# Kernel optimization log

Measured on AMD Instinct MI355X. Metric: run time of the kernel, lower is better.

Reference implementation:

```python
import jax, jax.numpy as jnp
import numpy as np

B, S, D, H, DH = 4, 2048, 1024, 16, 64

def setup_inputs() -> dict:
    key = jax.random.key(0)
    k1, k2, k3, k4, k5 = jax.random.split(key, 5)
    scale = 1.0 / np.sqrt(D)
    return {
        "x": jax.random.normal(k1, (B, S, D), dtype=jnp.float32),
        "w_qkv": jax.random.normal(k2, (D, 3, H, DH), dtype=jnp.float32) * scale,
        "b_qkv": jax.random.normal(k3, (3, H, DH), dtype=jnp.float32) * 0.02,
        "w_out": jax.random.normal(k4, (H, DH, D), dtype=jnp.float32) * (1.0 / np.sqrt(H * DH)),
        "b_out": jax.random.normal(k5, (D,), dtype=jnp.float32) * 0.02,
    }

def reference(x, w_qkv, b_qkv, w_out, b_out):
    # QKV projection: [B,S,D] x [D,3,H,Dh] -> [B,S,3,H,Dh]
    qkv = jnp.einsum('bsd,dthe->bsthe', x, w_qkv) + b_qkv
    q, k, v = qkv[:, :, 0], qkv[:, :, 1], qkv[:, :, 2]  # each [B,S,H,Dh]
    head_dim = q.shape[-1]
    # scores [B,H,Sq,Sk]
    scores = jnp.einsum('bqhe,bkhe->bhqk', q, k) / jnp.sqrt(jnp.float32(head_dim))
    seq = scores.shape[-1]
    causal = (jnp.arange(seq)[:, None] >= jnp.arange(seq)[None, :]).astype(scores.dtype)
    scores = scores - 1e9 * (1.0 - causal)  # additive mask as in source
    weights = jax.nn.softmax(scores, axis=-1)
    # dropout inactive (inference=True default)
    answers = jnp.einsum('bhqk,bkhe->bqhe', weights, v)  # [B,S,H,Dh]
    out = jnp.einsum('bqhe,hed->bqd', answers, w_out) + b_out
    return out
```

## Files before the change

kernel.cpp:

```cpp
#include <hip/hip_runtime.h>
#include <hip/hip_bf16.h>
#include <stdint.h>

#define B_    4
#define S_    2048
#define D_    1024
#define H_    16
#define DH_   64
#define M_TOT 8192
#define NQKV  3072
#define HDH   1024

typedef __bf16 bf16_t;
typedef bf16_t bf16x8 __attribute__((ext_vector_type(8)));
typedef float  f32x4  __attribute__((ext_vector_type(4)));
typedef float  f32x16 __attribute__((ext_vector_type(16)));

#define QSCALE 0.1803368801111204f

__device__ __forceinline__ short f2bf(float f) {
  union { float f; uint32_t u; } x; x.f = f;
  uint32_t r = (x.u + 0x7fffu + ((x.u >> 16) & 1u)) >> 16;
  return (short)(uint16_t)r;
}

__device__ __forceinline__ uint32_t cvt_pk_bf16(float lo, float hi) {
  uint32_t r;
  asm("v_cvt_pk_bf16_f32 %0, %1, %2" : "=v"(r) : "v"(lo), "v"(hi));
  return r;
}

__device__ __forceinline__ void permlane32_swap(uint32_t& d, uint32_t& s) {
  asm("v_permlane32_swap_b32 %0, %1" : "+v"(d), "+v"(s));
}

#define ASYNC_COPY16(g, l) \
  __builtin_amdgcn_global_load_lds((const __attribute__((address_space(1))) void*)(g), \
                                   (__attribute__((address_space(3))) void*)(l), 16, 0, 0)


__global__ __launch_bounds__(256) void k_cvt(const float* __restrict__ in, short* __restrict__ out, int n4) {
  int i = blockIdx.x * 256 + threadIdx.x;
  if (i < n4) {
    float4 v = ((const float4*)in)[i];
    short4 o;
    o.x = f2bf(v.x); o.y = f2bf(v.y); o.z = f2bf(v.z); o.w = f2bf(v.w);
    ((short4*)out)[i] = o;
  }
}

__global__ __launch_bounds__(256) void k_transpose_t(const float* __restrict__ in, short* __restrict__ out,
                                                     int R, int C) {
  __shared__ short t[32][33];
  const int bx = blockIdx.x * 32;
  const int by = blockIdx.y * 32;
  const int tid = threadIdx.x;
  const int row = tid >> 3, c4 = (tid & 7) * 4;
  const float4 v = *(const float4*)&in[(size_t)(by + row) * C + bx + c4];
  t[row][c4 + 0] = f2bf(v.x); t[row][c4 + 1] = f2bf(v.y);
  t[row][c4 + 2] = f2bf(v.z); t[row][c4 + 3] = f2bf(v.w);
  __syncthreads();
  short4 o;
  o.x = t[c4 + 0][row]; o.y = t[c4 + 1][row];
  o.z = t[c4 + 2][row]; o.w = t[c4 + 3][row];
  *(short4*)&out[(size_t)(bx + row) * R + by + c4] = o;
}


__device__ __forceinline__ void gemm_core(const short* __restrict__ A,
                                          const short* __restrict__ Bt,
                                          int row0, int col0, int K,
                                          short* lA, short* lB,
                                          f32x4 acc[4][4]) {
  const int tid  = threadIdx.x;
  const int wave = tid >> 6, lane = tid & 63;
  const int wr = wave >> 1, wc = wave & 1;
  const int stg_r = lane >> 2;
  const int stg_k = (lane & 3) * 8;
  const int fr = lane & 15;
  const int fk = (lane >> 4) * 8;

  for (int k0 = 0; k0 < K; k0 += 32) {
    __syncthreads();
#pragma unroll
    for (int c = 0; c < 2; ++c) {
      const int seg = wave * 2 + c;
      const short* ga = A  + (size_t)(row0 + seg * 16 + stg_r) * K + (k0 + stg_k);
      const short* gb = Bt + (size_t)(col0 + seg * 16 + stg_r) * K + (k0 + stg_k);
      ASYNC_COPY16(ga, lA + seg * 512);
      ASYNC_COPY16(gb, lB + seg * 512);
    }
    __syncthreads();
    bf16x8 af[4], bfr[4];
#pragma unroll
    for (int m = 0; m < 4; ++m)
      af[m] = *(const bf16x8*)(lA + (wr * 64 + m * 16 + fr) * 32 + fk);
#pragma unroll
    for (int n = 0; n < 4; ++n)
      bfr[n] = *(const bf16x8*)(lB + (wc * 64 + n * 16 + fr) * 32 + fk);
#pragma unroll
    for (int m = 0; m < 4; ++m)
#pragma unroll
      for (int n = 0; n < 4; ++n)
        acc[m][n] = __builtin_amdgcn_mfma_f32_16x16x32_bf16(af[m], bfr[n], acc[m][n], 0, 0, 0);
  }
}

__global__ __launch_bounds__(256) void k_gemm_qkv(const short* __restrict__ A, const short* __restrict__ Bt,
                                                  const float* __restrict__ bias,
                                                  short* __restrict__ Qb, short* __restrict__ Kb,
                                                  short* __restrict__ Vt) {
  __shared__ short lA[128 * 32];
  __shared__ short lB[128 * 32];
  f32x4 acc[4][4];
#pragma unroll
  for (int m = 0; m < 4; ++m)
#pragma unroll
    for (int n = 0; n < 4; ++n)
      acc[m][n] = (f32x4){0.f, 0.f, 0.f, 0.f};
  const int row0 = blockIdx.x * 128, col0 = blockIdx.y * 128;
  gemm_core(A, Bt, row0, col0, D_, lA, lB, acc);
  const int lane = threadIdx.x & 63, wave = threadIdx.x >> 6;
  const int wr = wave >> 1, wc = wave & 1;
#pragma unroll
  for (int m = 0; m < 4; ++m) {
    const int rbase = row0 + wr * 64 + m * 16 + (lane >> 4) * 4;
#pragma unroll
    for (int n = 0; n < 4; ++n) {
      const int col = col0 + wc * 64 + n * 16 + (lane & 15);
      const float bv = bias[col];
      const int t = col >> 10, rem = col & 1023, hh = rem >> 6, e = rem & 63;
#pragma unroll
      for (int r = 0; r < 4; ++r) {
        const int rw = rbase + r;
        const int bb = rw >> 11, s = rw & 2047;
        float v = acc[m][n][r] + bv;
        if (t == 0) {
          Qb[((size_t)(bb * H_ + hh) * S_ + s) * DH_ + e] = f2bf(v * QSCALE);
        } else if (t == 1) {
          Kb[((size_t)(bb * H_ + hh) * S_ + s) * DH_ + e] = f2bf(v);
        } else {
          Vt[((size_t)(bb * H_ + hh) * DH_ + e) * S_ + s] = f2bf(v);
        }
      }
    }
  }
}

__global__ __launch_bounds__(256) void k_gemm_out(const short* __restrict__ A, const short* __restrict__ Bt,
                                                  const float* __restrict__ bias, float* __restrict__ C) {
  __shared__ short lA[128 * 32];
  __shared__ short lB[128 * 32];
  f32x4 acc[4][4];
#pragma unroll
  for (int m = 0; m < 4; ++m)
#pragma unroll
    for (int n = 0; n < 4; ++n)
      acc[m][n] = (f32x4){0.f, 0.f, 0.f, 0.f};
  const int row0 = blockIdx.x * 128, col0 = blockIdx.y * 128;
  gemm_core(A, Bt, row0, col0, HDH, lA, lB, acc);
  const int lane = threadIdx.x & 63, wave = threadIdx.x >> 6;
  const int wr = wave >> 1, wc = wave & 1;
#pragma unroll
  for (int m = 0; m < 4; ++m) {
    const int rbase = row0 + wr * 64 + m * 16 + (lane >> 4) * 4;
#pragma unroll
    for (int n = 0; n < 4; ++n) {
      const int col = col0 + wc * 64 + n * 16 + (lane & 15);
      const float bv = bias[col];
#pragma unroll
      for (int r = 0; r < 4; ++r)
        C[(size_t)(rbase + r) * D_ + col] = acc[m][n][r] + bv;
    }
  }
}


template <bool MASKED>
__device__ __forceinline__ void softmax_pack(const f32x16& sacc, int ql, int hi,
                                             f32x16& o0, f32x16& o1,
                                             float& m, float& lsum,
                                             bf16x8& pb0v, bf16x8& pb1v) {
  float p[16];
#pragma unroll
  for (int r = 0; r < 16; ++r) {
    float s = sacc[r];
    if (MASKED) {
      const int kl = (r & 3) + 8 * (r >> 2) + 4 * hi;
      s = (kl <= ql) ? s : -1.0e30f;
    }
    p[r] = s;
  }
  float t0 = fmaxf(fmaxf(p[0], p[1]), p[2]);
  float t1 = fmaxf(fmaxf(p[3], p[4]), p[5]);
  float t2 = fmaxf(fmaxf(p[6], p[7]), p[8]);
  float t3 = fmaxf(fmaxf(p[9], p[10]), p[11]);
  float t4 = fmaxf(fmaxf(p[12], p[13]), p[14]);
  float pmax = fmaxf(fmaxf(fmaxf(t0, t1), t2), fmaxf(fmaxf(t3, t4), p[15]));
  if (__any(pmax - m > 8.0f)) {
    const float pmr = fmaxf(pmax, __shfl_xor(pmax, 32));
    const float mn = fmaxf(m, pmr);
    const float al = __builtin_amdgcn_exp2f(m - mn);
    lsum *= al;
#pragma unroll
    for (int r = 0; r < 16; ++r) { o0[r] *= al; o1[r] *= al; }
    m = mn;
  }
#pragma unroll
  for (int r = 0; r < 16; ++r) p[r] = __builtin_amdgcn_exp2f(p[r] - m);
  {
    float s0 = (p[0] + p[1]) + (p[2] + p[3]);
    float s1 = (p[4] + p[5]) + (p[6] + p[7]);
    float s2 = (p[8] + p[9]) + (p[10] + p[11]);
    float s3 = (p[12] + p[13]) + (p[14] + p[15]);
    lsum += (s0 + s1) + (s2 + s3);
  }
  uint32_t A0 = cvt_pk_bf16(p[0],  p[1]);
  uint32_t A1 = cvt_pk_bf16(p[2],  p[3]);
  uint32_t B0 = cvt_pk_bf16(p[4],  p[5]);
  uint32_t B1 = cvt_pk_bf16(p[6],  p[7]);
  uint32_t A2 = cvt_pk_bf16(p[8],  p[9]);
  uint32_t A3 = cvt_pk_bf16(p[10], p[11]);
  uint32_t B2 = cvt_pk_bf16(p[12], p[13]);
  uint32_t B3 = cvt_pk_bf16(p[14], p[15]);
  permlane32_swap(A0, B0);
  permlane32_swap(A1, B1);
  permlane32_swap(A2, B2);
  permlane32_swap(A3, B3);
  union { uint32_t u[4]; bf16x8 v; } pb0, pb1;
  pb0.u[0] = A0; pb0.u[1] = A1; pb0.u[2] = B0; pb0.u[3] = B1;
  pb1.u[0] = A2; pb1.u[1] = A3; pb1.u[2] = B2; pb1.u[3] = B3;
  pb0v = pb0.v; pb1v = pb1.v;
}

template <bool MASKED>
__device__ __forceinline__ void attn_tile(int kt, int ql, int hi,
                                          const short* __restrict__ Kp,
                                          const short* __restrict__ Vp,
                                          const bf16x8 qf[4],
                                          f32x16& oacc0, f32x16& oacc1,
                                          float& m, float& lsum) {
  const short* kb = Kp + (size_t)(kt + ql) * DH_ + hi * 8;
  bf16x8 kf0 = *(const bf16x8*)(kb);
  bf16x8 kf1 = *(const bf16x8*)(kb + 16);
  bf16x8 kf2 = *(const bf16x8*)(kb + 32);
  bf16x8 kf3 = *(const bf16x8*)(kb + 48);
  const short* vb0 = Vp + (size_t)(ql) * S_ + kt + hi * 8;
  const short* vb1 = Vp + (size_t)(32 + ql) * S_ + kt + hi * 8;
  bf16x8 vf00 = *(const bf16x8*)(vb0);
  bf16x8 vf01 = *(const bf16x8*)(vb0 + 16);
  bf16x8 vf10 = *(const bf16x8*)(vb1);
  bf16x8 vf11 = *(const bf16x8*)(vb1 + 16);

  f32x16 sacc;
#pragma unroll
  for (int r = 0; r < 16; ++r) sacc[r] = 0.f;
  __builtin_amdgcn_s_setprio(1);
  sacc = __builtin_amdgcn_mfma_f32_32x32x16_bf16(kf0, qf[0], sacc, 0, 0, 0);
  sacc = __builtin_amdgcn_mfma_f32_32x32x16_bf16(kf1, qf[1], sacc, 0, 0, 0);
  sacc = __builtin_amdgcn_mfma_f32_32x32x16_bf16(kf2, qf[2], sacc, 0, 0, 0);
  sacc = __builtin_amdgcn_mfma_f32_32x32x16_bf16(kf3, qf[3], sacc, 0, 0, 0);
  __builtin_amdgcn_s_setprio(0);

  bf16x8 pb0, pb1;
  softmax_pack<MASKED>(sacc, ql, hi, oacc0, oacc1, m, lsum, pb0, pb1);

  __builtin_amdgcn_s_setprio(1);
  oacc0 = __builtin_amdgcn_mfma_f32_32x32x16_bf16(vf00, pb0, oacc0, 0, 0, 0);
  oacc0 = __builtin_amdgcn_mfma_f32_32x32x16_bf16(vf01, pb1, oacc0, 0, 0, 0);
  oacc1 = __builtin_amdgcn_mfma_f32_32x32x16_bf16(vf10, pb0, oacc1, 0, 0, 0);
  oacc1 = __builtin_amdgcn_mfma_f32_32x32x16_bf16(vf11, pb1, oacc1, 0, 0, 0);
  __builtin_amdgcn_s_setprio(0);
}

template <bool MASKA>
__device__ __forceinline__ void attn_tile2(int kt, int ql, int hi,
                                           const short* __restrict__ Kp,
                                           const short* __restrict__ Vp,
                                           const bf16x8 qfA[4], const bf16x8 qfB[4],
                                           f32x16& oA0, f32x16& oA1, float& mA, float& lA,
                                           f32x16& oB0, f32x16& oB1, float& mB, float& lB) {
  const short* kb = Kp + (size_t)(kt + ql) * DH_ + hi * 8;
  bf16x8 kf0 = *(const bf16x8*)(kb);
  bf16x8 kf1 = *(const bf16x8*)(kb + 16);
  bf16x8 kf2 = *(const bf16x8*)(kb + 32);
  bf16x8 kf3 = *(const bf16x8*)(kb + 48);
  const short* vb0 = Vp + (size_t)(ql) * S_ + kt + hi * 8;
  const short* vb1 = Vp + (size_t)(32 + ql) * S_ + kt + hi * 8;
  bf16x8 vf00 = *(const bf16x8*)(vb0);
  bf16x8 vf01 = *(const bf16x8*)(vb0 + 16);
  bf16x8 vf10 = *(const bf16x8*)(vb1);
  bf16x8 vf11 = *(const bf16x8*)(vb1 + 16);

  f32x16 sA, sB;
#pragma unroll
  for (int r = 0; r < 16; ++r) { sA[r] = 0.f; sB[r] = 0.f; }
  __builtin_amdgcn_s_setprio(1);
  sA = __builtin_amdgcn_mfma_f32_32x32x16_bf16(kf0, qfA[0], sA, 0, 0, 0);
  sB = __builtin_amdgcn_mfma_f32_32x32x16_bf16(kf0, qfB[0], sB, 0, 0, 0);
  sA = __builtin_amdgcn_mfma_f32_32x32x16_bf16(kf1, qfA[1], sA, 0, 0, 0);
  sB = __builtin_amdgcn_mfma_f32_32x32x16_bf16(kf1, qfB[1], sB, 0, 0, 0);
  sA = __builtin_amdgcn_mfma_f32_32x32x16_bf16(kf2, qfA[2], sA, 0, 0, 0);
  sB = __builtin_amdgcn_mfma_f32_32x32x16_bf16(kf2, qfB[2], sB, 0, 0, 0);
  sA = __builtin_amdgcn_mfma_f32_32x32x16_bf16(kf3, qfA[3], sA, 0, 0, 0);
  sB = __builtin_amdgcn_mfma_f32_32x32x16_bf16(kf3, qfB[3], sB, 0, 0, 0);
  __builtin_amdgcn_s_setprio(0);

  bf16x8 pA0, pA1, pB0, pB1;
  softmax_pack<MASKA>(sA, ql, hi, oA0, oA1, mA, lA, pA0, pA1);
  softmax_pack<false>(sB, ql, hi, oB0, oB1, mB, lB, pB0, pB1);

  __builtin_amdgcn_s_setprio(1);
  oA0 = __builtin_amdgcn_mfma_f32_32x32x16_bf16(vf00, pA0, oA0, 0, 0, 0);
  oB0 = __builtin_amdgcn_mfma_f32_32x32x16_bf16(vf00, pB0, oB0, 0, 0, 0);
  oA0 = __builtin_amdgcn_mfma_f32_32x32x16_bf16(vf01, pA1, oA0, 0, 0, 0);
  oB0 = __builtin_amdgcn_mfma_f32_32x32x16_bf16(vf01, pB1, oB0, 0, 0, 0);
  oA1 = __builtin_amdgcn_mfma_f32_32x32x16_bf16(vf10, pA0, oA1, 0, 0, 0);
  oB1 = __builtin_amdgcn_mfma_f32_32x32x16_bf16(vf10, pB0, oB1, 0, 0, 0);
  oA1 = __builtin_amdgcn_mfma_f32_32x32x16_bf16(vf11, pA1, oA1, 0, 0, 0);
  oB1 = __builtin_amdgcn_mfma_f32_32x32x16_bf16(vf11, pB1, oB1, 0, 0, 0);
  __builtin_amdgcn_s_setprio(0);
}

__device__ __forceinline__ void write_out(short* __restrict__ att, int b, int h,
                                          int q0, int ql, int hi,
                                          const f32x16& o0, const f32x16& o1, float lsum) {
  lsum += __shfl_xor(lsum, 32);
  const float rl = __builtin_amdgcn_rcpf(lsum);
  short* ob = att + (size_t)((size_t)b * S_ + q0 + ql) * HDH + h * DH_ + 4 * hi;
#pragma unroll
  for (int dt = 0; dt < 2; ++dt) {
#pragma unroll
    for (int a = 0; a < 4; ++a) {
      const int rb = 4 * a;
      float v0 = (dt ? o1[rb + 0] : o0[rb + 0]) * rl;
      float v1 = (dt ? o1[rb + 1] : o0[rb + 1]) * rl;
      float v2 = (dt ? o1[rb + 2] : o0[rb + 2]) * rl;
      float v3 = (dt ? o1[rb + 3] : o0[rb + 3]) * rl;
      short4 o;
      o.x = f2bf(v0); o.y = f2bf(v1); o.z = f2bf(v2); o.w = f2bf(v3);
      *(short4*)(ob + dt * 32 + 8 * a) = o;
    }
  }
}

__global__ __launch_bounds__(64, 3) void k_attn(const short* __restrict__ Qb, const short* __restrict__ Kb,
                                                const short* __restrict__ Vt, short* __restrict__ att) {
  const int lane = threadIdx.x & 63;
  const int j = blockIdx.x;
  const int xcd = j & 7, c = j >> 3;
  const int bhLo = c & 7;
  const int s = 31 - (c >> 3);
  const int gg = xcd + 8 * bhLo;
  const int b = gg >> 4, h = gg & 15;
  const int pA = 2 * s, pB = 2 * s + 1;
  const int qA = pA * 32, qB = pB * 32;
  const size_t bh = (size_t)(b * H_ + h);
  const short* Qp = Qb + bh * (S_ * DH_);
  const short* Kp = Kb + bh * (S_ * DH_);
  const short* Vp = Vt + bh * (DH_ * S_);
  const int ql = lane & 31, hi = lane >> 5;

  bf16x8 qfA[4], qfB[4];
#pragma unroll
  for (int ss = 0; ss < 4; ++ss) {
    qfA[ss] = *(const bf16x8*)(Qp + (size_t)(qA + ql) * DH_ + ss * 16 + hi * 8);
    qfB[ss] = *(const bf16x8*)(Qp + (size_t)(qB + ql) * DH_ + ss * 16 + hi * 8);
  }

  f32x16 oA0, oA1, oB0, oB1;
#pragma unroll
  for (int r = 0; r < 16; ++r) { oA0[r] = 0.f; oA1[r] = 0.f; oB0[r] = 0.f; oB1[r] = 0.f; }
  float mA = -3.0e38f, lA = 0.f, mB = -3.0e38f, lB = 0.f;

#pragma unroll 1
  for (int t = 0; t < pA; ++t)
    attn_tile2<false>(t * 32, ql, hi, Kp, Vp, qfA, qfB, oA0, oA1, mA, lA, oB0, oB1, mB, lB);
  attn_tile2<true>(qA, ql, hi, Kp, Vp, qfA, qfB, oA0, oA1, mA, lA, oB0, oB1, mB, lB);
  attn_tile<true>(qB, ql, hi, Kp, Vp, qfB, oB0, oB1, mB, lB);

  write_out(att, b, h, qA, ql, hi, oA0, oA1, lA);
  write_out(att, b, h, qB, ql, hi, oB0, oB1, lB);
}


extern "C" void kernel_launch(void* const* d_in, const int* in_sizes, int n_in,
                              void* d_out, int out_size, void* d_ws, size_t ws_size,
                              hipStream_t stream) {
  const float* x     = (const float*)d_in[0];
  const float* w_qkv = (const float*)d_in[1];
  const float* b_qkv = (const float*)d_in[2];
  const float* w_out = (const float*)d_in[3];
  const float* b_out = (const float*)d_in[4];
  float* out = (float*)d_out;

  char* p = (char*)d_ws;
  short* xb    = (short*)p; p += (size_t)M_TOT * D_ * 2;
  short* wqkvT = (short*)p; p += (size_t)NQKV * D_ * 2;
  short* woutT = (short*)p; p += (size_t)D_ * HDH * 2;
  short* Qb    = (short*)p; p += (size_t)B_ * H_ * S_ * DH_ * 2;
  short* Kb    = (short*)p; p += (size_t)B_ * H_ * S_ * DH_ * 2;
  short* Vt    = (short*)p; p += (size_t)B_ * H_ * S_ * DH_ * 2;
  short* att   = (short*)p; p += (size_t)M_TOT * HDH * 2;

  k_cvt<<<M_TOT * D_ / 4 / 256, 256, 0, stream>>>(x, xb, M_TOT * D_ / 4);
  k_transpose_t<<<dim3(NQKV / 32, D_ / 32), 256, 0, stream>>>(w_qkv, wqkvT, D_, NQKV);
  k_transpose_t<<<dim3(D_ / 32, HDH / 32), 256, 0, stream>>>(w_out, woutT, HDH, D_);
  k_gemm_qkv<<<dim3(M_TOT / 128, NQKV / 128), 256, 0, stream>>>(xb, wqkvT, b_qkv, Qb, Kb, Vt);
  k_attn<<<2048, 64, 0, stream>>>(Qb, Kb, Vt, att);
  k_gemm_out<<<dim3(M_TOT / 128, D_ / 128), 256, 0, stream>>>(att, woutT, b_out, out);
}
```

Before: 202.9 us.

## Rewrite QKV GEMM with 256x256 tiles, double-buffered async LDS loads and swizzle

Replaces the QKV projection GEMM with a 512-thread kernel that computes 256x256 tiles using K-steps of 64. It double-buffers LDS, issuing async global-to-LDS loads for the next K-tile in two halves interleaved with MFMA phases. It XOR-swizzles the LDS layout to avoid bank conflicts and raises wave priority around MFMA bursts. The aim is to hide memory latency and raise arithmetic intensity, at the cost of much more LDS (128KB per block) and register pressure, which may limit occupancy.

```diff
diff --git a/kernel.cpp b/kernel.cpp
--- a/kernel.cpp
+++ b/kernel.cpp
@@ -37,6 +37,8 @@
 #define ASYNC_COPY16(g, l) \
   __builtin_amdgcn_global_load_lds((const __attribute__((address_space(1))) void*)(g), \
                                    (__attribute__((address_space(3))) void*)(l), 16, 0, 0)
+
+#define BARRIER() do { __builtin_amdgcn_sched_barrier(0); __builtin_amdgcn_s_barrier(); __builtin_amdgcn_sched_barrier(0); } while (0)
 
 
 __global__ __launch_bounds__(256) void k_cvt(const float* __restrict__ in, short* __restrict__ out, int n4) {
@@ -67,6 +69,172 @@
 }
 
 
+#define STAGE_HALF(bsel, kt, h) do {                                                        \
+    const short* gA0 = A  + (size_t)(row0 + (h) * 128 + srow     ) * 1024 + (kt) * 64 + scol; \
+    const short* gA1 = A  + (size_t)(row0 + (h) * 128 + srow + 64) * 1024 + (kt) * 64 + scol; \
+    const short* gB0 = Bt + (size_t)(col0 + (h) * 128 + srow     ) * 1024 + (kt) * 64 + scol; \
+    const short* gB1 = Bt + (size_t)(col0 + (h) * 128 + srow + 64) * 1024 + (kt) * 64 + scol; \
+    ASYNC_COPY16(gA0, lA + (bsel) * 16384 + (h) * 8192 + wave * 512);                         \
+    ASYNC_COPY16(gA1, lA + (bsel) * 16384 + (h) * 8192 + wave * 512 + 4096);                  \
+    ASYNC_COPY16(gB0, lB + (bsel) * 16384 + (h) * 8192 + wave * 512);                         \
+    ASYNC_COPY16(gB1, lB + (bsel) * 16384 + (h) * 8192 + wave * 512 + 4096);                  \
+  } while (0)
+
+__global__ __launch_bounds__(512, 2) void k_gemm_qkv(const short* __restrict__ A, const short* __restrict__ Bt,
+                                                     const float* __restrict__ bias,
+                                                     short* __restrict__ Qb, short* __restrict__ Kb,
+                                                     short* __restrict__ Vt) {
+  __shared__ short lA[2 * 256 * 64];
+  __shared__ short lB[2 * 256 * 64];
+  const int tid = threadIdx.x;
+  const int wave = tid >> 6, lane = tid & 63;
+  const int wr = wave >> 2, wc = wave & 3;
+  const int fr = lane & 15, hi16 = lane >> 4;
+  const int row0 = blockIdx.x * 256, col0 = blockIdx.y * 256;
+
+  const int srow = tid >> 3;
+  const int scol = ((tid & 7) ^ (srow & 7)) * 8;
+
+  const int cs0 = ((0 + hi16) ^ (fr & 7)) * 8;
+  const int cs1 = ((4 + hi16) ^ (fr & 7)) * 8;
+  const int rowA = (wr * 128 + fr) * 64;
+  const int rowB = (wc * 64 + fr) * 64;
+
+  f32x4 acc[8][4];
+#pragma unroll
+  for (int m = 0; m < 8; ++m)
+#pragma unroll
+    for (int n = 0; n < 4; ++n) acc[m][n] = (f32x4){0.f, 0.f, 0.f, 0.f};
+
+  STAGE_HALF(0, 0, 0);
+  STAGE_HALF(0, 0, 1);
+
+  bf16x8 bfrag[4][2];
+
+#pragma unroll 1
+  for (int t = 0; t < 16; ++t) {
+    const int cur = t & 1, nxt = cur ^ 1;
+    const int cb = cur * 16384;
+
+    if (t < 15) {
+      STAGE_HALF(nxt, t + 1, 0);
+      asm volatile("s_waitcnt vmcnt(4)" ::: "memory");
+    } else {
+      asm volatile("s_waitcnt vmcnt(0)" ::: "memory");
+    }
+    BARRIER();
+#pragma unroll
+    for (int n = 0; n < 4; ++n) {
+      bfrag[n][0] = *(const bf16x8*)(lB + cb + rowB + n * 1024 + cs0);
+      bfrag[n][1] = *(const bf16x8*)(lB + cb + rowB + n * 1024 + cs1);
+    }
+    {
+      bf16x8 af[2][2];
+#pragma unroll
+      for (int im = 0; im < 2; ++im) {
+        af[im][0] = *(const bf16x8*)(lA + cb + rowA + (0 + im) * 1024 + cs0);
+        af[im][1] = *(const bf16x8*)(lA + cb + rowA + (0 + im) * 1024 + cs1);
+      }
+      __builtin_amdgcn_s_setprio(1);
+#pragma unroll
+      for (int im = 0; im < 2; ++im)
+#pragma unroll
+        for (int n = 0; n < 4; ++n) {
+          acc[0 + im][n] = __builtin_amdgcn_mfma_f32_16x16x32_bf16(af[im][0], bfrag[n][0], acc[0 + im][n], 0, 0, 0);
+          acc[0 + im][n] = __builtin_amdgcn_mfma_f32_16x16x32_bf16(af[im][1], bfrag[n][1], acc[0 + im][n], 0, 0, 0);
+        }
+      __builtin_amdgcn_s_setprio(0);
+    }
+    BARRIER();
+
+    {
+      bf16x8 af[2][2];
+#pragma unroll
+      for (int im = 0; im < 2; ++im) {
+        af[im][0] = *(const bf16x8*)(lA + cb + rowA + (2 + im) * 1024 + cs0);
+        af[im][1] = *(const bf16x8*)(lA + cb + rowA + (2 + im) * 1024 + cs1);
+      }
+      if (t < 15) STAGE_HALF(nxt, t + 1, 1);
+      BARRIER();
+      __builtin_amdgcn_s_setprio(1);
+#pragma unroll
+      for (int im = 0; im < 2; ++im)
+#pragma unroll
+        for (int n = 0; n < 4; ++n) {
+          acc[2 + im][n] = __builtin_amdgcn_mfma_f32_16x16x32_bf16(af[im][0], bfrag[n][0], acc[2 + im][n], 0, 0, 0);
+          acc[2 + im][n] = __builtin_amdgcn_mfma_f32_16x16x32_bf16(af[im][1], bfrag[n][1], acc[2 + im][n], 0, 0, 0);
+        }
+      __builtin_amdgcn_s_setprio(0);
+    }
+    BARRIER();
+
+    {
+      bf16x8 af[2][2];
+#pragma unroll
+      for (int im = 0; im < 2; ++im) {
+        af[im][0] = *(const bf16x8*)(lA + cb + rowA + (4 + im) * 1024 + cs0);
+        af[im][1] = *(const bf16x8*)(lA + cb + rowA + (4 + im) * 1024 + cs1);
+      }
+      BARRIER();
+      __builtin_amdgcn_s_setprio(1);
+#pragma unroll
+      for (int im = 0; im < 2; ++im)
+#pragma unroll
+        for (int n = 0; n < 4; ++n) {
+          acc[4 + im][n] = __builtin_amdgcn_mfma_f32_16x16x32_bf16(af[im][0], bfrag[n][0], acc[4 + im][n], 0, 0, 0);
+          acc[4 + im][n] = __builtin_amdgcn_mfma_f32_16x16x32_bf16(af[im][1], bfrag[n][1], acc[4 + im][n], 0, 0, 0);
+        }
+      __builtin_amdgcn_s_setprio(0);
+    }
+    BARRIER();
+
+    {
+      bf16x8 af[2][2];
+#pragma unroll
+      for (int im = 0; im < 2; ++im) {
+        af[im][0] = *(const bf16x8*)(lA + cb + rowA + (6 + im) * 1024 + cs0);
+        af[im][1] = *(const bf16x8*)(lA + cb + rowA + (6 + im) * 1024 + cs1);
+      }
+      BARRIER();
+      __builtin_amdgcn_s_setprio(1);
+#pragma unroll
+      for (int im = 0; im < 2; ++im)
+#pragma unroll
+        for (int n = 0; n < 4; ++n) {
+          acc[6 + im][n] = __builtin_amdgcn_mfma_f32_16x16x32_bf16(af[im][0], bfrag[n][0], acc[6 + im][n], 0, 0, 0);
+          acc[6 + im][n] = __builtin_amdgcn_mfma_f32_16x16x32_bf16(af[im][1], bfrag[n][1], acc[6 + im][n], 0, 0, 0);
+        }
+      __builtin_amdgcn_s_setprio(0);
+    }
+    BARRIER();
+  }
+
+#pragma unroll
+  for (int m = 0; m < 8; ++m) {
+    const int rbase = row0 + wr * 128 + m * 16 + hi16 * 4;
+#pragma unroll
+    for (int n = 0; n < 4; ++n) {
+      const int col = col0 + wc * 64 + n * 16 + fr;
+      const float bv = bias[col];
+      const int tt = col >> 10, rem = col & 1023, hh = rem >> 6, e = rem & 63;
+#pragma unroll
+      for (int r = 0; r < 4; ++r) {
+        const int rw = rbase + r;
+        const int bb = rw >> 11, s = rw & 2047;
+        float v = acc[m][n][r] + bv;
+        if (tt == 0) {
+          Qb[((size_t)(bb * H_ + hh) * S_ + s) * DH_ + e] = f2bf(v * QSCALE);
+        } else if (tt == 1) {
+          Kb[((size_t)(bb * H_ + hh) * S_ + s) * DH_ + e] = f2bf(v);
+        } else {
+          Vt[((size_t)(bb * H_ + hh) * DH_ + e) * S_ + s] = f2bf(v);
+        }
+      }
+    }
+  }
+}
+
+
 __device__ __forceinline__ void gemm_core(const short* __restrict__ A,
                                           const short* __restrict__ Bt,
                                           int row0, int col0, int K,
@@ -103,47 +271,6 @@
 #pragma unroll
       for (int n = 0; n < 4; ++n)
         acc[m][n] = __builtin_amdgcn_mfma_f32_16x16x32_bf16(af[m], bfr[n], acc[m][n], 0, 0, 0);
-  }
-}
-
-__global__ __launch_bounds__(256) void k_gemm_qkv(const short* __restrict__ A, const short* __restrict__ Bt,
-                                                  const float* __restrict__ bias,
-                                                  short* __restrict__ Qb, short* __restrict__ Kb,
-                                                  short* __restrict__ Vt) {
-  __shared__ short lA[128 * 32];
-  __shared__ short lB[128 * 32];
-  f32x4 acc[4][4];
-#pragma unroll
-  for (int m = 0; m < 4; ++m)
-#pragma unroll
-    for (int n = 0; n < 4; ++n)
-      acc[m][n] = (f32x4){0.f, 0.f, 0.f, 0.f};
-  const int row0 = blockIdx.x * 128, col0 = blockIdx.y * 128;
-  gemm_core(A, Bt, row0, col0, D_, lA, lB, acc);
-  const int lane = threadIdx.x & 63, wave = threadIdx.x >> 6;
-  const int wr = wave >> 1, wc = wave & 1;
-#pragma unroll
-  for (int m = 0; m < 4; ++m) {
-    const int rbase = row0 + wr * 64 + m * 16 + (lane >> 4) * 4;
-#pragma unroll
-    for (int n = 0; n < 4; ++n) {
-      const int col = col0 + wc * 64 + n * 16 + (lane & 15);
-      const float bv = bias[col];
-      const int t = col >> 10, rem = col & 1023, hh = rem >> 6, e = rem & 63;
-#pragma unroll
-      for (int r = 0; r < 4; ++r) {
-        const int rw = rbase + r;
-        const int bb = rw >> 11, s = rw & 2047;
-        float v = acc[m][n][r] + bv;
-        if (t == 0) {
-          Qb[((size_t)(bb * H_ + hh) * S_ + s) * DH_ + e] = f2bf(v * QSCALE);
-        } else if (t == 1) {
-          Kb[((size_t)(bb * H_ + hh) * S_ + s) * DH_ + e] = f2bf(v);
-        } else {
-          Vt[((size_t)(bb * H_ + hh) * DH_ + e) * S_ + s] = f2bf(v);
-        }
-      }
-    }
   }
 }
 
@@ -406,7 +533,7 @@
   k_cvt<<<M_TOT * D_ / 4 / 256, 256, 0, stream>>>(x, xb, M_TOT * D_ / 4);
   k_transpose_t<<<dim3(NQKV / 32, D_ / 32), 256, 0, stream>>>(w_qkv, wqkvT, D_, NQKV);
   k_transpose_t<<<dim3(D_ / 32, HDH / 32), 256, 0, stream>>>(w_out, woutT, HDH, D_);
-  k_gemm_qkv<<<dim3(M_TOT / 128, NQKV / 128), 256, 0, stream>>>(xb, wqkvT, b_qkv, Qb, Kb, Vt);
+  k_gemm_qkv<<<dim3(M_TOT / 256, NQKV / 256), 512, 0, stream>>>(xb, wqkvT, b_qkv, Qb, Kb, Vt);
   k_attn<<<2048, 64, 0, stream>>>(Qb, Kb, Vt, att);
   k_gemm_out<<<dim3(M_TOT / 128, D_ / 128), 256, 0, stream>>>(att, woutT, b_out, out);
 }
```

Result: slower. 226.9 us (+11.8%).
